# Performance work log

Measured on AMD Instinct MI355X. Metric: run time of the kernel, lower is better.

The kernel has to match this reference:

```python
import math
import jax, jax.numpy as jnp
import numpy as np

N_GRAPHS = 400
N_PER = 50
N = N_GRAPHS * N_PER          # 20000 nodes
K = 12                        # k_neighbors
E = N * K                     # 240000 edges
ND = 128                      # node_dim
TD = 128                      # time_dim
LD = 128                      # latent_dim
SD = 32                       # species_emb_dim
L = 4                         # num_layers


def _lin(key, fi, fo):
    return (jax.random.normal(key, (fi, fo), dtype=jnp.float32) / np.sqrt(fi)).astype(jnp.float32)


def setup_inputs() -> dict:
    rng = np.random.default_rng(0)
    coords = (rng.standard_normal((N_GRAPHS, N_PER, 3)) * 3.0).astype(np.float32)
    # exact kNN per graph (loop=False): dst = center node, src = neighbor
    d = ((coords[:, :, None, :] - coords[:, None, :, :]) ** 2).sum(-1)  # [G, n, n]
    ii = np.arange(N_PER)
    d[:, ii, ii] = np.inf
    nbr = np.argpartition(d, K, axis=-1)[:, :, :K]                      # [G, n, K]
    base = (np.arange(N_GRAPHS) * N_PER)[:, None, None]
    edge_src = (nbr + base).reshape(-1).astype(np.int64)
    edge_dst = (np.broadcast_to(ii[None, :, None], (N_GRAPHS, N_PER, K)) + base).reshape(-1).astype(np.int64)
    batch_indices = np.repeat(np.arange(N_GRAPHS), N_PER).astype(np.int64)

    key = jax.random.key(0)
    ks = jax.random.split(key, 32)
    inp = {
        'z_nodes': jax.random.normal(ks[0], (N, LD), dtype=jnp.float32),
        't': jax.random.uniform(ks[1], (N_GRAPHS,), dtype=jnp.float32) * 1000.0,
        'cart_coords': jnp.asarray(coords.reshape(N, 3)),
        'species': jax.random.randint(ks[2], (N,), 1, 119),
        'batch_indices': jnp.asarray(batch_indices),
        'edge_src': jnp.asarray(edge_src),
        'edge_dst': jnp.asarray(edge_dst),
        # parameters
        'species_emb': jax.random.normal(ks[3], (119, SD), dtype=jnp.float32),
        'tm_W1': _lin(ks[4], TD, 2 * TD), 'tm_b1': jnp.zeros((2 * TD,), jnp.float32),
        'tm_W2': _lin(ks[5], 2 * TD, TD), 'tm_b2': jnp.zeros((TD,), jnp.float32),
        'ne_W': _lin(ks[6], LD + SD, ND), 'ne_b': jnp.zeros((ND,), jnp.float32),
        'eW1': jnp.stack([_lin(jax.random.fold_in(ks[7], l), 2 * ND + 1 + TD, ND) for l in range(L)]),
        'eb1': jnp.zeros((L, ND), jnp.float32),
        'eW2': jnp.stack([_lin(jax.random.fold_in(ks[8], l), ND, ND) for l in range(L)]),
        'eb2': jnp.zeros((L, ND), jnp.float32),
        'cW1': jnp.stack([_lin(jax.random.fold_in(ks[9], l), ND, ND) for l in range(L)]),
        'cb1': jnp.zeros((L, ND), jnp.float32),
        'cW2': jnp.stack([_lin(jax.random.fold_in(ks[10], l), ND, 1) for l in range(L)]),
        'nW1': jnp.stack([_lin(jax.random.fold_in(ks[11], l), 2 * ND + TD, ND) for l in range(L)]),
        'nb1': jnp.zeros((L, ND), jnp.float32),
        'nW2': jnp.stack([_lin(jax.random.fold_in(ks[12], l), ND, ND) for l in range(L)]),
        'nb2': jnp.zeros((L, ND), jnp.float32),
    }
    return inp


def reference(z_nodes, t, cart_coords, species, batch_indices, edge_src, edge_dst,
              species_emb, tm_W1, tm_b1, tm_W2, tm_b2, ne_W, ne_b,
              eW1, eb1, eW2, eb2, cW1, cb1, cW2, nW1, nb1, nW2, nb2):
    silu = jax.nn.silu
    # sinusoidal time embedding + time MLP
    half = TD // 2
    freqs = jnp.exp(jnp.arange(half, dtype=jnp.float32) * (-math.log(10000.0) / (half - 1)))
    ang = t[:, None] * freqs[None, :]                     # [G, half]
    temb = jnp.concatenate([jnp.sin(ang), jnp.cos(ang)], axis=-1)
    temb = silu(temb @ tm_W1 + tm_b1) @ tm_W2 + tm_b2     # [G, TD]
    t_nodes = temb[batch_indices]                         # [N, TD]

    sp = species_emb[species]                             # [N, SD]
    h = jnp.concatenate([z_nodes, sp], axis=-1) @ ne_W + ne_b  # [N, ND]

    diff = cart_coords[edge_src] - cart_coords[edge_dst]  # [E, 3]
    dist_sq = jnp.sum(diff * diff, axis=-1, keepdims=True)  # [E, 1]
    dist = jnp.sqrt(dist_sq + 1e-8)
    t_edges = t_nodes[edge_src]                           # [E, TD]

    n = h.shape[0]
    total_shift = jnp.zeros_like(cart_coords)
    for l in range(L):
        edge_in = jnp.concatenate([h[edge_src], h[edge_dst], dist_sq, t_edges], axis=-1)
        m = silu(edge_in @ eW1[l] + eb1[l])
        m = silu(m @ eW2[l] + eb2[l])                     # [E, ND]
        gate = silu(m @ cW1[l] + cb1[l]) @ cW2[l]         # [E, 1]
        shift = diff / dist * gate                        # [E, 3]
        total_shift = total_shift + jax.ops.segment_sum(shift, edge_dst, num_segments=n)
        m_i = jax.ops.segment_sum(m, edge_dst, num_segments=n)  # [N, ND]
        node_in = jnp.concatenate([h, m_i, t_nodes], axis=-1)
        h = h + (silu(node_in @ nW1[l] + nb1[l]) @ nW2[l] + nb2[l])
    return (total_shift, h)
```

## Files before the change

### kernel.cpp

```cpp
#include <hip/hip_runtime.h>
#include <math.h>

#define GN 400
#define NPER 50
#define NN 20000
#define LL 4

typedef __attribute__((ext_vector_type(8))) short short8;
typedef __attribute__((ext_vector_type(4))) float f32x4;

__device__ __forceinline__ float fast_rcp(float x) {
#if __has_builtin(__builtin_amdgcn_rcpf)
  return __builtin_amdgcn_rcpf(x);
#else
  return 1.0f / x;
#endif
}
__device__ __forceinline__ float silu_f(float x) {
  return x * fast_rcp(1.0f + __expf(-x));
}
__device__ __forceinline__ unsigned short f2bu(float f) {
  unsigned int u = __float_as_uint(f);
  unsigned int r = (u + 0x7fffu + ((u >> 16) & 1u)) >> 16;
  return (unsigned short)r;
}
__device__ __forceinline__ unsigned int pack2bf(float lo, float hi) {
  return (unsigned int)f2bu(lo) | ((unsigned int)f2bu(hi) << 16);
}
__device__ __forceinline__ float bhi(unsigned int u) { return __uint_as_float(u & 0xffff0000u); }
__device__ __forceinline__ float blo(unsigned int u) { return __uint_as_float(u << 16); }

__device__ __forceinline__ short8 pack8(const float* v) {
  union { unsigned int u[4]; short8 s; } t;
  t.u[0] = pack2bf(v[0], v[1]);
  t.u[1] = pack2bf(v[2], v[3]);
  t.u[2] = pack2bf(v[4], v[5]);
  t.u[3] = pack2bf(v[6], v[7]);
  return t.s;
}

__global__ __launch_bounds__(128) void time_kernel(
    const float* __restrict__ t,
    const float* __restrict__ tm_W1, const float* __restrict__ tm_b1,
    const float* __restrict__ tm_W2, const float* __restrict__ tm_b2,
    const float* __restrict__ eW1, const float* __restrict__ eb1,
    const float* __restrict__ nW1, const float* __restrict__ nb1,
    float* __restrict__ temb, float* __restrict__ tE, float* __restrict__ tN)
{
  int g = blockIdx.x;
  int j = threadIdx.x;
  __shared__ float x[128];
  __shared__ float hid[256];
  __shared__ float te[128];
  float tv = t[g];
  if (j < 64) {
    float f = __expf((float)j * (-9.210340371976184f / 63.0f));
    float a = tv * f;
    x[j] = sinf(a);
    x[j + 64] = cosf(a);
  }
  __syncthreads();
  for (int o = j; o < 256; o += 128) {
    float acc = tm_b1[o];
    for (int k = 0; k < 128; ++k) acc = fmaf(x[k], tm_W1[k * 256 + o], acc);
    hid[o] = silu_f(acc);
  }
  __syncthreads();
  {
    float acc = tm_b2[j];
    for (int k = 0; k < 256; ++k) acc = fmaf(hid[k], tm_W2[k * 128 + j], acc);
    te[j] = acc;
    temb[g * 128 + j] = acc;
  }
  __syncthreads();
  for (int l = 0; l < LL; ++l) {
    const float* W = eW1 + (l * 385 + 257) * 128;
    float acc = eb1[l * 128 + j];
    for (int k = 0; k < 128; ++k) acc = fmaf(te[k], W[k * 128 + j], acc);
    tE[(l * GN + g) * 128 + j] = acc;
    const float* Wn = nW1 + (l * 384 + 256) * 128;
    float acc2 = nb1[l * 128 + j];
    for (int k = 0; k < 128; ++k) acc2 = fmaf(te[k], Wn[k * 128 + j], acc2);
    tN[(l * GN + g) * 128 + j] = acc2;
  }
}

__global__ __launch_bounds__(256) void prep_transpose(
    const float* __restrict__ eW1, const float* __restrict__ eW2,
    const float* __restrict__ cW1, const float* __restrict__ nW1,
    const float* __restrict__ nW2, const float* __restrict__ ne_W,
    unsigned short* __restrict__ eABt, unsigned short* __restrict__ eW2t,
    unsigned short* __restrict__ cW1t, unsigned short* __restrict__ nW1t,
    unsigned short* __restrict__ nW2t, unsigned short* __restrict__ ne_Wt)
{
  __shared__ float tile[32][33];
  int j = blockIdx.y;
  const float* src;
  unsigned short* dst;
  int dstride = 128, Kj = 128;
  if (j < 28) {
    int l = j / 7, m = j % 7;
    switch (m) {
      case 0: src = eW1 + (l * 385 + 0) * 128;   dst = eABt + l * 256 * 128;             break;
      case 1: src = eW1 + (l * 385 + 128) * 128; dst = eABt + l * 256 * 128 + 128 * 128; break;
      case 2: src = eW2 + l * 16384;             dst = eW2t + l * 16384;                 break;
      case 3: src = cW1 + l * 16384;             dst = cW1t + l * 16384;                 break;
      case 4: src = nW1 + (l * 384 + 0) * 128;   dst = nW1t + l * 128 * 256; dstride = 256; break;
      case 5: src = nW1 + (l * 384 + 128) * 128; dst = nW1t + l * 128 * 256 + 128; dstride = 256; break;
      default: src = nW2 + l * 16384;            dst = nW2t + l * 16384;                 break;
    }
  } else {
    src = ne_W; dst = ne_Wt; dstride = 160; Kj = 160;
  }
  int gx = blockIdx.x;
  int tk = (gx % 5) * 32;
  int tn = (gx / 5) * 32;
  if (tk >= Kj) return;
  int ti = threadIdx.x >> 5, tj = threadIdx.x & 31;
#pragma unroll
  for (int p = 0; p < 4; ++p) {
    int i = ti + p * 8;
    tile[i][tj] = src[(tk + i) * 128 + tn + tj];
  }
  __syncthreads();
#pragma unroll
  for (int p = 0; p < 4; ++p) {
    int i = ti + p * 8;
    dst[(tn + i) * dstride + tk + tj] = f2bu(tile[tj][i]);
  }
}

__global__ __launch_bounds__(64) void edge_mfma(
    const unsigned short* __restrict__ hAB,
    const float* __restrict__ coords, const int* __restrict__ edge_src,
    const float* __restrict__ eW1,
    const unsigned short* __restrict__ eW2t, const float* __restrict__ eb2,
    const unsigned short* __restrict__ cW1t, const float* __restrict__ cb1,
    const float* __restrict__ cW2, const float* __restrict__ tE,
    unsigned short* __restrict__ m_i, float* __restrict__ shift_out,
    int l, int addflag)
{
  __shared__ unsigned short mbuf[48 * 136];
  __shared__ float sdir[48 * 4];
  __shared__ float sgate[48];

  int l6 = threadIdx.x;
  int e16 = l6 & 15, q = l6 >> 4;
  int nbase = blockIdx.x * 4;
  int ebase = blockIdx.x * 48;

  const unsigned short* eW2t_l = eW2t + l * 16384;
  const unsigned short* cW1t_l = cW1t + l * 16384;
  const float* eb2_l = eb2 + l * 128;
  const float* cb1_l = cb1 + l * 128;
  const float* cW2_l = cW2 + l * 128;
  const float* tE_l = tE + l * GN * 128;
  const float* wd = eW1 + (l * 385 + 256) * 128;

  int ssrc[3], sdst[3];
  float sds[3];
#pragma unroll
  for (int grp = 0; grp < 3; ++grp) {
    int eloc = grp * 16 + e16;
    int e = ebase + eloc;
    int src = edge_src[e];
    src = min(max(src, 0), NN - 1);
    int dst = nbase + eloc / 12;
    float dx = coords[src * 3 + 0] - coords[dst * 3 + 0];
    float dy = coords[src * 3 + 1] - coords[dst * 3 + 1];
    float dz = coords[src * 3 + 2] - coords[dst * 3 + 2];
    float ds = dx * dx + dy * dy + dz * dz;
    float rinv = 1.0f / sqrtf(ds + 1e-8f);
    if (q == 0) {
      sdir[eloc * 4 + 0] = dx * rinv;
      sdir[eloc * 4 + 1] = dy * rinv;
      sdir[eloc * 4 + 2] = dz * rinv;
    }
    ssrc[grp] = src; sdst[grp] = dst; sds[grp] = ds;
  }

  short8 bfr[3][4];
#pragma unroll
  for (int grp = 0; grp < 3; ++grp) {
    int g = sdst[grp] / NPER;
    float ds = sds[grp];
#pragma unroll
    for (int kc = 0; kc < 4; ++kc) {
      int k0 = kc * 32 + q * 8;
      uint4 ua = *(const uint4*)(hAB + ssrc[grp] * 256 + k0);
      uint4 ub = *(const uint4*)(hAB + sdst[grp] * 256 + 128 + k0);
      float4 w0 = *(const float4*)(wd + k0);
      float4 w1 = *(const float4*)(wd + k0 + 4);
      float4 t0 = *(const float4*)(tE_l + g * 128 + k0);
      float4 t1 = *(const float4*)(tE_l + g * 128 + k0 + 4);
      float v[8];
      v[0] = silu_f(blo(ua.x) + blo(ub.x) + ds * w0.x + t0.x);
      v[1] = silu_f(bhi(ua.x) + bhi(ub.x) + ds * w0.y + t0.y);
      v[2] = silu_f(blo(ua.y) + blo(ub.y) + ds * w0.z + t0.z);
      v[3] = silu_f(bhi(ua.y) + bhi(ub.y) + ds * w0.w + t0.w);
      v[4] = silu_f(blo(ua.z) + blo(ub.z) + ds * w1.x + t1.x);
      v[5] = silu_f(bhi(ua.z) + bhi(ub.z) + ds * w1.y + t1.y);
      v[6] = silu_f(blo(ua.w) + blo(ub.w) + ds * w1.z + t1.z);
      v[7] = silu_f(bhi(ua.w) + bhi(ub.w) + ds * w1.w + t1.w);
      bfr[grp][kc] = pack8(v);
    }
  }

#pragma unroll
  for (int mt = 0; mt < 8; ++mt) {
    short8 af[4];
#pragma unroll
    for (int kc = 0; kc < 4; ++kc)
      af[kc] = *(const short8*)(eW2t_l + (mt * 16 + e16) * 128 + kc * 32 + q * 8);
    f32x4 acc[3] = {(f32x4){0,0,0,0}, (f32x4){0,0,0,0}, (f32x4){0,0,0,0}};
#pragma unroll
    for (int kc = 0; kc < 4; ++kc) {
#pragma unroll
      for (int grp = 0; grp < 3; ++grp)
        acc[grp] = __builtin_amdgcn_mfma_f32_16x16x32_bf16(af[kc], bfr[grp][kc], acc[grp], 0, 0, 0);
    }
    float4 b4 = *(const float4*)(eb2_l + mt * 16 + q * 4);
#pragma unroll
    for (int grp = 0; grp < 3; ++grp) {
      float v0 = silu_f(acc[grp][0] + b4.x);
      float v1 = silu_f(acc[grp][1] + b4.y);
      float v2 = silu_f(acc[grp][2] + b4.z);
      float v3 = silu_f(acc[grp][3] + b4.w);
      uint2 p;
      p.x = pack2bf(v0, v1);
      p.y = pack2bf(v2, v3);
      *(uint2*)&mbuf[(grp * 16 + e16) * 136 + mt * 16 + q * 4] = p;
    }
  }
  __syncthreads();

  short8 af2[3][4];
#pragma unroll
  for (int grp = 0; grp < 3; ++grp)
#pragma unroll
    for (int kc = 0; kc < 4; ++kc)
      af2[grp][kc] = *(const short8*)&mbuf[(grp * 16 + e16) * 136 + kc * 32 + q * 8];

  float gp[3][4] = {{0,0,0,0},{0,0,0,0},{0,0,0,0}};
#pragma unroll
  for (int ct = 0; ct < 8; ++ct) {
    short8 bf[4];
#pragma unroll
    for (int kc = 0; kc < 4; ++kc)
      bf[kc] = *(const short8*)(cW1t_l + (ct * 16 + e16) * 128 + kc * 32 + q * 8);
    f32x4 acc[3] = {(f32x4){0,0,0,0}, (f32x4){0,0,0,0}, (f32x4){0,0,0,0}};
#pragma unroll
    for (int kc = 0; kc < 4; ++kc) {
#pragma unroll
      for (int grp = 0; grp < 3; ++grp)
        acc[grp] = __builtin_amdgcn_mfma_f32_16x16x32_bf16(af2[grp][kc], bf[kc], acc[grp], 0, 0, 0);
    }
    float cb = cb1_l[ct * 16 + e16];
    float c2 = cW2_l[ct * 16 + e16];
#pragma unroll
    for (int grp = 0; grp < 3; ++grp)
#pragma unroll
      for (int r = 0; r < 4; ++r)
        gp[grp][r] += silu_f(acc[grp][r] + cb) * c2;
  }
#pragma unroll
  for (int grp = 0; grp < 3; ++grp)
#pragma unroll
    for (int r = 0; r < 4; ++r) {
      float v = gp[grp][r];
      v += __shfl_xor(v, 1);
      v += __shfl_xor(v, 2);
      v += __shfl_xor(v, 4);
      v += __shfl_xor(v, 8);
      if (e16 == 0) sgate[grp * 16 + q * 4 + r] = v;
    }
  __syncthreads();

  {
    int nl = q, c8 = e16 * 8;
    float s[8] = {0,0,0,0,0,0,0,0};
#pragma unroll
    for (int r = 0; r < 12; ++r) {
      uint4 u = *(const uint4*)&mbuf[(nl * 12 + r) * 136 + c8];
      s[0] += blo(u.x); s[1] += bhi(u.x);
      s[2] += blo(u.y); s[3] += bhi(u.y);
      s[4] += blo(u.z); s[5] += bhi(u.z);
      s[6] += blo(u.w); s[7] += bhi(u.w);
    }
    uint4 o;
    o.x = pack2bf(s[0], s[1]); o.y = pack2bf(s[2], s[3]);
    o.z = pack2bf(s[4], s[5]); o.w = pack2bf(s[6], s[7]);
    *(uint4*)(m_i + (nbase + nl) * 128 + c8) = o;
  }
  if (l6 < 12) {
    int nl = l6 / 3, c = l6 - nl * 3;
    float s = 0.f;
#pragma unroll
    for (int r = 0; r < 12; ++r) {
      int e = nl * 12 + r;
      s = fmaf(sdir[e * 4 + c], sgate[e], s);
    }
    int n = nbase + nl;
    if (addflag) shift_out[n * 3 + c] += s;
    else         shift_out[n * 3 + c] = s;
  }
}

__global__ __launch_bounds__(64) void node_mfma(
    float* __restrict__ h, const unsigned short* __restrict__ m_i,
    const unsigned short* __restrict__ nW1t_l, const unsigned short* __restrict__ nW2t_l,
    const float* __restrict__ nb2_l, const float* __restrict__ tN_l,
    const unsigned short* __restrict__ eABt_next, unsigned short* __restrict__ hAB,
    int has_c)
{
  __shared__ unsigned short z1buf[16 * 136];
  __shared__ unsigned short hbuf[16 * 136];
  int l6 = threadIdx.x, e16 = l6 & 15, q = l6 >> 4;
  int row = blockIdx.x * 16 + e16;
  int g = row / NPER;

  short8 bfh[8];
#pragma unroll
  for (int kc = 0; kc < 8; ++kc) {
    int k0 = kc * 32 + q * 8;
    if (k0 < 128) {
      float4 f0 = *(const float4*)(h + row * 128 + k0);
      float4 f1 = *(const float4*)(h + row * 128 + k0 + 4);
      float v[8] = {f0.x, f0.y, f0.z, f0.w, f1.x, f1.y, f1.z, f1.w};
      bfh[kc] = pack8(v);
    } else {
      bfh[kc] = *(const short8*)(m_i + row * 128 + (k0 - 128));
    }
  }
#pragma unroll
  for (int mt = 0; mt < 8; ++mt) {
    short8 af[8];
#pragma unroll
    for (int kc = 0; kc < 8; ++kc)
      af[kc] = *(const short8*)(nW1t_l + (mt * 16 + e16) * 256 + kc * 32 + q * 8);
    f32x4 acc = (f32x4){0,0,0,0};
#pragma unroll
    for (int kc = 0; kc < 8; ++kc)
      acc = __builtin_amdgcn_mfma_f32_16x16x32_bf16(af[kc], bfh[kc], acc, 0, 0, 0);
    float4 tv = *(const float4*)(tN_l + g * 128 + mt * 16 + q * 4);
    float v0 = silu_f(acc[0] + tv.x);
    float v1 = silu_f(acc[1] + tv.y);
    float v2 = silu_f(acc[2] + tv.z);
    float v3 = silu_f(acc[3] + tv.w);
    uint2 p; p.x = pack2bf(v0, v1); p.y = pack2bf(v2, v3);
    *(uint2*)&z1buf[e16 * 136 + mt * 16 + q * 4] = p;
  }
  __syncthreads();

  short8 zf[4];
#pragma unroll
  for (int kc = 0; kc < 4; ++kc)
    zf[kc] = *(const short8*)&z1buf[e16 * 136 + kc * 32 + q * 8];
#pragma unroll
  for (int mt = 0; mt < 8; ++mt) {
    short8 af[4];
#pragma unroll
    for (int kc = 0; kc < 4; ++kc)
      af[kc] = *(const short8*)(nW2t_l + (mt * 16 + e16) * 128 + kc * 32 + q * 8);
    f32x4 acc = (f32x4){0,0,0,0};
#pragma unroll
    for (int kc = 0; kc < 4; ++kc)
      acc = __builtin_amdgcn_mfma_f32_16x16x32_bf16(af[kc], zf[kc], acc, 0, 0, 0);
    float4 hv = *(const float4*)(h + row * 128 + mt * 16 + q * 4);
    float4 b4 = *(const float4*)(nb2_l + mt * 16 + q * 4);
    float4 o;
    o.x = hv.x + acc[0] + b4.x;
    o.y = hv.y + acc[1] + b4.y;
    o.z = hv.z + acc[2] + b4.z;
    o.w = hv.w + acc[3] + b4.w;
    *(float4*)(h + row * 128 + mt * 16 + q * 4) = o;
    uint2 p; p.x = pack2bf(o.x, o.y); p.y = pack2bf(o.z, o.w);
    *(uint2*)&hbuf[e16 * 136 + mt * 16 + q * 4] = p;
  }
  if (has_c) {
    __syncthreads();
    short8 hf[4];
#pragma unroll
    for (int kc = 0; kc < 4; ++kc)
      hf[kc] = *(const short8*)&hbuf[e16 * 136 + kc * 32 + q * 8];
#pragma unroll
    for (int mt = 0; mt < 16; ++mt) {
      short8 af[4];
#pragma unroll
      for (int kc = 0; kc < 4; ++kc)
        af[kc] = *(const short8*)(eABt_next + (mt * 16 + e16) * 128 + kc * 32 + q * 8);
      f32x4 acc = (f32x4){0,0,0,0};
#pragma unroll
      for (int kc = 0; kc < 4; ++kc)
        acc = __builtin_amdgcn_mfma_f32_16x16x32_bf16(af[kc], hf[kc], acc, 0, 0, 0);
      uint2 p; p.x = pack2bf(acc[0], acc[1]); p.y = pack2bf(acc[2], acc[3]);
      *(uint2*)(hAB + row * 256 + mt * 16 + q * 4) = p;
    }
  }
}

__global__ __launch_bounds__(64) void encoder_mfma(
    const float* __restrict__ z, const int* __restrict__ species,
    const float* __restrict__ species_emb,
    const unsigned short* __restrict__ ne_Wt, const float* __restrict__ ne_b,
    const unsigned short* __restrict__ eABt0,
    float* __restrict__ h, unsigned short* __restrict__ hAB)
{
  __shared__ unsigned short hbuf[16 * 136];
  int l6 = threadIdx.x, e16 = l6 & 15, q = l6 >> 4;
  int row = blockIdx.x * 16 + e16;
  int sp = species[row];
  sp = min(max(sp, 0), 118);

  short8 bfh[5];
#pragma unroll
  for (int kc = 0; kc < 5; ++kc) {
    int k0 = kc * 32 + q * 8;
    const float* src = (k0 < 128) ? (z + row * 128 + k0)
                                  : (species_emb + sp * 32 + (k0 - 128));
    float4 f0 = *(const float4*)src;
    float4 f1 = *(const float4*)(src + 4);
    float v[8] = {f0.x, f0.y, f0.z, f0.w, f1.x, f1.y, f1.z, f1.w};
    bfh[kc] = pack8(v);
  }
#pragma unroll
  for (int mt = 0; mt < 8; ++mt) {
    short8 af[5];
#pragma unroll
    for (int kc = 0; kc < 5; ++kc)
      af[kc] = *(const short8*)(ne_Wt + (mt * 16 + e16) * 160 + kc * 32 + q * 8);
    f32x4 acc = (f32x4){0,0,0,0};
#pragma unroll
    for (int kc = 0; kc < 5; ++kc)
      acc = __builtin_amdgcn_mfma_f32_16x16x32_bf16(af[kc], bfh[kc], acc, 0, 0, 0);
    float4 b4 = *(const float4*)(ne_b + mt * 16 + q * 4);
    float4 o;
    o.x = acc[0] + b4.x; o.y = acc[1] + b4.y;
    o.z = acc[2] + b4.z; o.w = acc[3] + b4.w;
    *(float4*)(h + row * 128 + mt * 16 + q * 4) = o;
    uint2 p; p.x = pack2bf(o.x, o.y); p.y = pack2bf(o.z, o.w);
    *(uint2*)&hbuf[e16 * 136 + mt * 16 + q * 4] = p;
  }
  __syncthreads();
  short8 hf[4];
#pragma unroll
  for (int kc = 0; kc < 4; ++kc)
    hf[kc] = *(const short8*)&hbuf[e16 * 136 + kc * 32 + q * 8];
#pragma unroll
  for (int mt = 0; mt < 16; ++mt) {
    short8 af[4];
#pragma unroll
    for (int kc = 0; kc < 4; ++kc)
      af[kc] = *(const short8*)(eABt0 + (mt * 16 + e16) * 128 + kc * 32 + q * 8);
    f32x4 acc = (f32x4){0,0,0,0};
#pragma unroll
    for (int kc = 0; kc < 4; ++kc)
      acc = __builtin_amdgcn_mfma_f32_16x16x32_bf16(af[kc], hf[kc], acc, 0, 0, 0);
    uint2 p; p.x = pack2bf(acc[0], acc[1]); p.y = pack2bf(acc[2], acc[3]);
    *(uint2*)(hAB + row * 256 + mt * 16 + q * 4) = p;
  }
}

extern "C" void kernel_launch(void* const* d_in, const int* in_sizes, int n_in,
                              void* d_out, int out_size, void* d_ws, size_t ws_size,
                              hipStream_t stream)
{
  const float* z_nodes     = (const float*)d_in[0];
  const float* t           = (const float*)d_in[1];
  const float* coords      = (const float*)d_in[2];
  const int*   species     = (const int*)d_in[3];
  const int*   edge_src    = (const int*)d_in[5];
  const float* species_emb = (const float*)d_in[7];
  const float* tm_W1 = (const float*)d_in[8];
  const float* tm_b1 = (const float*)d_in[9];
  const float* tm_W2 = (const float*)d_in[10];
  const float* tm_b2 = (const float*)d_in[11];
  const float* ne_W  = (const float*)d_in[12];
  const float* ne_b  = (const float*)d_in[13];
  const float* eW1   = (const float*)d_in[14];
  const float* eb1   = (const float*)d_in[15];
  const float* eW2   = (const float*)d_in[16];
  const float* eb2   = (const float*)d_in[17];
  const float* cW1   = (const float*)d_in[18];
  const float* cb1   = (const float*)d_in[19];
  const float* cW2   = (const float*)d_in[20];
  const float* nW1   = (const float*)d_in[21];
  const float* nb1   = (const float*)d_in[22];
  const float* nW2   = (const float*)d_in[23];
  const float* nb2   = (const float*)d_in[24];

  char* wsb = (char*)d_ws;
  float* temb = (float*)(wsb + 0);
  float* tEb  = (float*)(wsb + 204800);
  float* tNb  = (float*)(wsb + 1024000);
  unsigned short* hAB  = (unsigned short*)(wsb + 1843200);
  unsigned short* m_i  = (unsigned short*)(wsb + 12083200);
  unsigned short* eABt = (unsigned short*)(wsb + 17203200);
  unsigned short* eW2t = (unsigned short*)(wsb + 17465344);
  unsigned short* cW1t = (unsigned short*)(wsb + 17596416);
  unsigned short* nW1t = (unsigned short*)(wsb + 17727488);
  unsigned short* nW2t = (unsigned short*)(wsb + 17989632);
  unsigned short* ne_Wt= (unsigned short*)(wsb + 18120704);

  float* outp  = (float*)d_out;
  float* shift = outp;
  float* h     = outp + 60000;

  time_kernel<<<GN, 128, 0, stream>>>(t, tm_W1, tm_b1, tm_W2, tm_b2,
                                      eW1, eb1, nW1, nb1, temb, tEb, tNb);
  prep_transpose<<<dim3(20, 29), 256, 0, stream>>>(eW1, eW2, cW1, nW1, nW2, ne_W,
                                                   eABt, eW2t, cW1t, nW1t, nW2t, ne_Wt);
  encoder_mfma<<<NN / 16, 64, 0, stream>>>(z_nodes, species, species_emb,
                                           ne_Wt, ne_b, eABt, h, hAB);
  for (int l = 0; l < LL; ++l) {
    edge_mfma<<<NN / 4, 64, 0, stream>>>(hAB, coords, edge_src, eW1,
                                         eW2t, eb2, cW1t, cb1, cW2, tEb,
                                         m_i, shift, l, (l > 0) ? 1 : 0);
    int has_c = (l < LL - 1) ? 1 : 0;
    node_mfma<<<NN / 16, 64, 0, stream>>>(h, m_i,
                                          nW1t + l * 128 * 256, nW2t + l * 16384,
                                          nb2 + l * 128, tNb + l * GN * 128,
                                          has_c ? (eABt + (l + 1) * 256 * 128) : eABt,
                                          hAB, has_c);
  }
}
```

Before: 550.3 us.

## Fold time embedding into hAB precompute and use cheaper bf16 packing

The per-graph time-embedding term of the first edge layer is now added once per node, into the destination half of hAB, inside the encoder and node kernels. The edge kernel therefore no longer loads tE vectors for every edge. The edge kernel also interchanges its loops so the distance-weight loads are hoisted out of the per-group loop. It also swaps round-to-nearest-even bf16 conversion for a cheaper add-and-perm rounding. The trade-off is that the time term is now rounded into bf16 together with hB, and ties round differently, so numerics shift slightly.

```diff
diff --git a/kernel.cpp b/kernel.cpp
--- a/kernel.cpp
+++ b/kernel.cpp
@@ -27,6 +27,15 @@
 __device__ __forceinline__ unsigned int pack2bf(float lo, float hi) {
   return (unsigned int)f2bu(lo) | ((unsigned int)f2bu(hi) << 16);
 }
+__device__ __forceinline__ unsigned int pack2bf_fast(float lo, float hi) {
+  unsigned int a = __float_as_uint(lo) + 0x8000u;
+  unsigned int b = __float_as_uint(hi) + 0x8000u;
+#if __has_builtin(__builtin_amdgcn_perm)
+  return __builtin_amdgcn_perm(b, a, 0x07060302);
+#else
+  return (b & 0xffff0000u) | (a >> 16);
+#endif
+}
 __device__ __forceinline__ float bhi(unsigned int u) { return __uint_as_float(u & 0xffff0000u); }
 __device__ __forceinline__ float blo(unsigned int u) { return __uint_as_float(u << 16); }
 
@@ -36,6 +45,14 @@
   t.u[1] = pack2bf(v[2], v[3]);
   t.u[2] = pack2bf(v[4], v[5]);
   t.u[3] = pack2bf(v[6], v[7]);
+  return t.s;
+}
+__device__ __forceinline__ short8 pack8_fast(const float* v) {
+  union { unsigned int u[4]; short8 s; } t;
+  t.u[0] = pack2bf_fast(v[0], v[1]);
+  t.u[1] = pack2bf_fast(v[2], v[3]);
+  t.u[2] = pack2bf_fast(v[4], v[5]);
+  t.u[3] = pack2bf_fast(v[6], v[7]);
   return t.s;
 }
 
@@ -136,7 +153,7 @@
     const float* __restrict__ eW1,
     const unsigned short* __restrict__ eW2t, const float* __restrict__ eb2,
     const unsigned short* __restrict__ cW1t, const float* __restrict__ cb1,
-    const float* __restrict__ cW2, const float* __restrict__ tE,
+    const float* __restrict__ cW2,
     unsigned short* __restrict__ m_i, float* __restrict__ shift_out,
     int l, int addflag)
 {
@@ -154,7 +171,6 @@
   const float* eb2_l = eb2 + l * 128;
   const float* cb1_l = cb1 + l * 128;
   const float* cW2_l = cW2 + l * 128;
-  const float* tE_l = tE + l * GN * 128;
   const float* wd = eW1 + (l * 385 + 256) * 128;
 
   int ssrc[3], sdst[3];
@@ -181,28 +197,25 @@
 
   short8 bfr[3][4];
 #pragma unroll
-  for (int grp = 0; grp < 3; ++grp) {
-    int g = sdst[grp] / NPER;
-    float ds = sds[grp];
-#pragma unroll
-    for (int kc = 0; kc < 4; ++kc) {
-      int k0 = kc * 32 + q * 8;
+  for (int kc = 0; kc < 4; ++kc) {
+    int k0 = kc * 32 + q * 8;
+    float4 w0 = *(const float4*)(wd + k0);
+    float4 w1 = *(const float4*)(wd + k0 + 4);
+#pragma unroll
+    for (int grp = 0; grp < 3; ++grp) {
+      float ds = sds[grp];
       uint4 ua = *(const uint4*)(hAB + ssrc[grp] * 256 + k0);
       uint4 ub = *(const uint4*)(hAB + sdst[grp] * 256 + 128 + k0);
-      float4 w0 = *(const float4*)(wd + k0);
-      float4 w1 = *(const float4*)(wd + k0 + 4);
-      float4 t0 = *(const float4*)(tE_l + g * 128 + k0);
-      float4 t1 = *(const float4*)(tE_l + g * 128 + k0 + 4);
       float v[8];
-      v[0] = silu_f(blo(ua.x) + blo(ub.x) + ds * w0.x + t0.x);
-      v[1] = silu_f(bhi(ua.x) + bhi(ub.x) + ds * w0.y + t0.y);
-      v[2] = silu_f(blo(ua.y) + blo(ub.y) + ds * w0.z + t0.z);
-      v[3] = silu_f(bhi(ua.y) + bhi(ub.y) + ds * w0.w + t0.w);
-      v[4] = silu_f(blo(ua.z) + blo(ub.z) + ds * w1.x + t1.x);
-      v[5] = silu_f(bhi(ua.z) + bhi(ub.z) + ds * w1.y + t1.y);
-      v[6] = silu_f(blo(ua.w) + blo(ub.w) + ds * w1.z + t1.z);
-      v[7] = silu_f(bhi(ua.w) + bhi(ub.w) + ds * w1.w + t1.w);
-      bfr[grp][kc] = pack8(v);
+      v[0] = silu_f(blo(ua.x) + blo(ub.x) + ds * w0.x);
+      v[1] = silu_f(bhi(ua.x) + bhi(ub.x) + ds * w0.y);
+      v[2] = silu_f(blo(ua.y) + blo(ub.y) + ds * w0.z);
+      v[3] = silu_f(bhi(ua.y) + bhi(ub.y) + ds * w0.w);
+      v[4] = silu_f(blo(ua.z) + blo(ub.z) + ds * w1.x);
+      v[5] = silu_f(bhi(ua.z) + bhi(ub.z) + ds * w1.y);
+      v[6] = silu_f(blo(ua.w) + blo(ub.w) + ds * w1.z);
+      v[7] = silu_f(bhi(ua.w) + bhi(ub.w) + ds * w1.w);
+      bfr[grp][kc] = pack8_fast(v);
     }
   }
 
@@ -227,8 +240,8 @@
       float v2 = silu_f(acc[grp][2] + b4.z);
       float v3 = silu_f(acc[grp][3] + b4.w);
       uint2 p;
-      p.x = pack2bf(v0, v1);
-      p.y = pack2bf(v2, v3);
+      p.x = pack2bf_fast(v0, v1);
+      p.y = pack2bf_fast(v2, v3);
       *(uint2*)&mbuf[(grp * 16 + e16) * 136 + mt * 16 + q * 4] = p;
     }
   }
@@ -288,8 +301,8 @@
       s[6] += blo(u.w); s[7] += bhi(u.w);
     }
     uint4 o;
-    o.x = pack2bf(s[0], s[1]); o.y = pack2bf(s[2], s[3]);
-    o.z = pack2bf(s[4], s[5]); o.w = pack2bf(s[6], s[7]);
+    o.x = pack2bf_fast(s[0], s[1]); o.y = pack2bf_fast(s[2], s[3]);
+    o.z = pack2bf_fast(s[4], s[5]); o.w = pack2bf_fast(s[6], s[7]);
     *(uint4*)(m_i + (nbase + nl) * 128 + c8) = o;
   }
   if (l6 < 12) {
@@ -310,8 +323,8 @@
     float* __restrict__ h, const unsigned short* __restrict__ m_i,
     const unsigned short* __restrict__ nW1t_l, const unsigned short* __restrict__ nW2t_l,
     const float* __restrict__ nb2_l, const float* __restrict__ tN_l,
-    const unsigned short* __restrict__ eABt_next, unsigned short* __restrict__ hAB,
-    int has_c)
+    const unsigned short* __restrict__ eABt_next, const float* __restrict__ tE_next,
+    unsigned short* __restrict__ hAB, int has_c)
 {
   __shared__ unsigned short z1buf[16 * 136];
   __shared__ unsigned short hbuf[16 * 136];
@@ -393,6 +406,10 @@
 #pragma unroll
       for (int kc = 0; kc < 4; ++kc)
         acc = __builtin_amdgcn_mfma_f32_16x16x32_bf16(af[kc], hf[kc], acc, 0, 0, 0);
+      if (mt >= 8) {
+        float4 tv = *(const float4*)(tE_next + g * 128 + (mt - 8) * 16 + q * 4);
+        acc[0] += tv.x; acc[1] += tv.y; acc[2] += tv.z; acc[3] += tv.w;
+      }
       uint2 p; p.x = pack2bf(acc[0], acc[1]); p.y = pack2bf(acc[2], acc[3]);
       *(uint2*)(hAB + row * 256 + mt * 16 + q * 4) = p;
     }
@@ -403,12 +420,13 @@
     const float* __restrict__ z, const int* __restrict__ species,
     const float* __restrict__ species_emb,
     const unsigned short* __restrict__ ne_Wt, const float* __restrict__ ne_b,
-    const unsigned short* __restrict__ eABt0,
+    const unsigned short* __restrict__ eABt0, const float* __restrict__ tE0,
     float* __restrict__ h, unsigned short* __restrict__ hAB)
 {
   __shared__ unsigned short hbuf[16 * 136];
   int l6 = threadIdx.x, e16 = l6 & 15, q = l6 >> 4;
   int row = blockIdx.x * 16 + e16;
+  int g = row / NPER;
   int sp = species[row];
   sp = min(max(sp, 0), 118);
 
@@ -456,6 +474,10 @@
 #pragma unroll
     for (int kc = 0; kc < 4; ++kc)
       acc = __builtin_amdgcn_mfma_f32_16x16x32_bf16(af[kc], hf[kc], acc, 0, 0, 0);
+    if (mt >= 8) {
+      float4 tv = *(const float4*)(tE0 + g * 128 + (mt - 8) * 16 + q * 4);
+      acc[0] += tv.x; acc[1] += tv.y; acc[2] += tv.z; acc[3] += tv.w;
+    }
     uint2 p; p.x = pack2bf(acc[0], acc[1]); p.y = pack2bf(acc[2], acc[3]);
     *(uint2*)(hAB + row * 256 + mt * 16 + q * 4) = p;
   }
@@ -511,16 +533,17 @@
   prep_transpose<<<dim3(20, 29), 256, 0, stream>>>(eW1, eW2, cW1, nW1, nW2, ne_W,
                                                    eABt, eW2t, cW1t, nW1t, nW2t, ne_Wt);
   encoder_mfma<<<NN / 16, 64, 0, stream>>>(z_nodes, species, species_emb,
-                                           ne_Wt, ne_b, eABt, h, hAB);
+                                           ne_Wt, ne_b, eABt, tEb, h, hAB);
   for (int l = 0; l < LL; ++l) {
     edge_mfma<<<NN / 4, 64, 0, stream>>>(hAB, coords, edge_src, eW1,
-                                         eW2t, eb2, cW1t, cb1, cW2, tEb,
+                                         eW2t, eb2, cW1t, cb1, cW2,
                                          m_i, shift, l, (l > 0) ? 1 : 0);
     int has_c = (l < LL - 1) ? 1 : 0;
     node_mfma<<<NN / 16, 64, 0, stream>>>(h, m_i,
                                           nW1t + l * 128 * 256, nW2t + l * 16384,
                                           nb2 + l * 128, tNb + l * GN * 128,
                                           has_c ? (eABt + (l + 1) * 256 * 128) : eABt,
+                                          has_c ? (tEb + (l + 1) * GN * 128) : tEb,
                                           hAB, has_c);
   }
 }
```

Result: faster. 532.1 us (-3.3%).
